# Optimization experiments

Measured on AMD Instinct MI355X. Metric: run time of the kernel, lower is better.

## Reference

```python
import jax, jax.numpy as jnp
import numpy as np

B, T, I, H, O = 128, 64, 512, 1024, 512
EPS = 0.01
N_MAX = 12  # static max ACT ponder steps per timestep (halts at ~2 steps at init)


def setup_inputs() -> dict:
    key = jax.random.key(0)
    ks = jax.random.split(key, 10)
    k = 1.0 / np.sqrt(H)
    u = lambda kk, shape: jax.random.uniform(kk, shape, jnp.float32, -k, k)
    return {
        "x": jax.random.normal(ks[0], (B, T, I), jnp.float32),
        "s0": jax.random.normal(ks[1], (1, B, H), jnp.float32) * 0.1,
        "w_ih": u(ks[2], (H, 1 + I)),
        "w_hh": u(ks[3], (H, H)),
        "b_ih": u(ks[4], (H,)),
        "b_hh": u(ks[5], (H,)),
        "w_halt": u(ks[6], (1, H)),
        "b_halt": u(ks[7], (1,)),
        "w_out": u(ks[8], (O, H)),
        "b_out": u(ks[9], (O,)),
    }


def _binarize_st(p):
    # Binarize autograd.Function: forward -> 1 where p > 0 (sigmoid outputs are
    # always positive, zeroed halted entries stay 0); backward -> identity (STE).
    return p + jax.lax.stop_gradient(jnp.where(p > 0, 1.0, 0.0) - p)


def reference(x, s0, w_ih, w_hh, b_ih, b_hh, w_halt, b_halt, w_out, b_out):
    def cell(inp, h):  # inp [B,1+I], h [B,H] -> tanh RNN cell
        return jnp.tanh(inp @ w_ih.T + b_ih + h @ w_hh.T + b_hh)

    def timestep(h_carry, x_t):  # h_carry [B,H], x_t [B,I]
        ones = jnp.ones((B, 1), x_t.dtype)
        x1 = jnp.concatenate([ones, x_t], axis=1)          # flag=1: first ponder step
        x0 = jnp.concatenate([ones * 0.0, x_t], axis=1)    # flag=0: continued pondering
        # ponder step 0 (always contributes for every sample)
        h = cell(x1, h_carry)
        out = h @ w_out.T + b_out                 # [B,O]
        p = jax.nn.sigmoid(h @ w_halt.T + b_halt) # [B,1]
        w = _binarize_st(p)
        out_acc = out * w
        h_acc = h * w
        cum = p[:, 0]
        # ponder value is only assigned when a sample halts at step 0 (original bug kept)
        pond = jnp.where(cum >= 1.0 - EPS, 2.0, 0.0)

        def ponder_step(carry, _):
            h_prev, cum, out_acc, h_acc = carry
            active = (cum < 1.0 - EPS).astype(h_prev.dtype)[:, None]  # [B,1]
            h = cell(x0, h_prev) * active
            out = (h @ w_out.T + b_out) * active
            p = jax.nn.sigmoid(h @ w_halt.T + b_halt) * active
            w = _binarize_st(p)
            return (h, cum + p[:, 0], out_acc + out * w, h_acc + h * w), None

        (h, cum, out_acc, h_acc), _ = jax.lax.scan(
            ponder_step, (h, cum, out_acc, h_acc), None, length=N_MAX - 1)
        # next-timestep hidden is the binarized-weight accumulation of states
        return h_acc, (out_acc, pond)

    h_last, (outputs, ponder) = jax.lax.scan(timestep, s0[0], jnp.swapaxes(x, 0, 1))
    return jnp.swapaxes(outputs, 0, 1), jnp.swapaxes(ponder, 0, 1)  # [B,T,O], [B,T]
```

## Files before the change

kernel.cpp:

```cpp
#include <hip/hip_runtime.h>
#include <hip/hip_cooperative_groups.h>
#include <math.h>

namespace cg = cooperative_groups;

#define NB 128
#define NT 64
#define NI 512
#define NH 1024
#define NO 512
#define PONDOFF (NB*NT*NO)

extern __shared__ float smem[];

__device__ __forceinline__ void group_barrier(unsigned* ctr, unsigned target, int tid)
{
    __syncthreads();
    if (tid == 0) {
        __hip_atomic_fetch_add(ctr, 1u, __ATOMIC_RELEASE, __HIP_MEMORY_SCOPE_AGENT);
        while (__hip_atomic_load(ctr, __ATOMIC_RELAXED, __HIP_MEMORY_SCOPE_AGENT) < target)
            __builtin_amdgcn_s_sleep(1);
    }
    if (tid < 64)
        __builtin_amdgcn_fence(__ATOMIC_ACQUIRE, "agent");
    __syncthreads();
}

__global__ void __launch_bounds__(1024, 1)
arnn_coop(const float* __restrict__ x, const float* __restrict__ s0,
          const float* __restrict__ w_ih, const float* __restrict__ w_hh,
          const float* __restrict__ b_ih, const float* __restrict__ b_hh,
          const float* __restrict__ w_halt, const float* __restrict__ b_halt,
          const float* __restrict__ w_out, const float* __restrict__ b_out,
          float* __restrict__ out, float* __restrict__ ws)
{
    cg::grid_group grid = cg::this_grid();
    const int tid = threadIdx.x;
    const int bid = blockIdx.x;
    const int gid = bid * 1024 + tid;

    float* wihT  = ws;
    float* hbuf  = wihT + NI*NH;
    float* habuf = hbuf + NB*2*NH;
    unsigned* ctrA = (unsigned*)(habuf + 2*NB*NH);

    const int gp = bid >> 5, lb = bid & 31;

    __shared__ float s_whalt[NH + (NH/16)*4];
    __shared__ int   s_t[16];
    __shared__ float s_cum[16];
    __shared__ int   s_n[16];
    __shared__ int   s_et[16], s_en[16];
    __shared__ unsigned char s_sl[16];
    __shared__ unsigned char s_run[16];
    __shared__ unsigned char s_mode[16];
    __shared__ unsigned char s_epi[16];

    for (int e = gid; e < NI*NH; e += 256*1024) {
        const int i = e >> 10, jj = e & 1023;
        wihT[e] = w_ih[jj*(NI+1) + 1 + i];
    }
    if (gid < 8*32)
        __hip_atomic_store(&ctrA[gid], 0u, __ATOMIC_RELAXED, __HIP_MEMORY_SCOPE_AGENT);
    for (int e = tid; e < 1024*32; e += 1024) {
        const int k = e & 1023, jj = e >> 10;
        const float v = w_hh[(lb*32 + jj)*NH + k];
        const int su = (jj >> 1) ^ ((k >> 6) & 15);
        smem[k*32 + su*2 + (jj & 1)] = v;
    }
    {
        const int j = tid;
        s_whalt[j + ((j >> 4) << 2)] = w_halt[j];
    }
    if (tid < 16) {
        s_t[tid] = 0; s_cum[tid] = 0.0f; s_n[tid] = 0;
        s_et[tid] = 0; s_en[tid] = 0;
        s_sl[tid] = 0; s_run[tid] = 1; s_mode[tid] = 0; s_epi[tid] = 0;
    }
    grid.sync();

    unsigned* ctr = ctrA + gp*32;

    const int w    = tid >> 6;
    const int lane = tid & 63;
    const int rq   = w >> 2;
    const int co   = w & 3;
    const int up   = lane & 3;
    const int ks   = lane >> 2;
    const int u    = co*4 + up;
    const int jg   = lb*32 + u*2;
    const int b0   = gp*16 + rq*4;
    const bool k0  = (ks == 0);
    const int ldsb = ks*2048 + ((u ^ ks) << 1);

    const float bh  = b_halt[0];
    const float bias0 = k0 ? (b_ih[jg]   + b_hh[jg])   : 0.0f;
    const float bias1 = k0 ? (b_ih[jg+1] + b_hh[jg+1]) : 0.0f;
    const float w0a   = k0 ? w_ih[jg*(NI+1)]     : 0.0f;
    const float w0b   = k0 ? w_ih[(jg+1)*(NI+1)] : 0.0f;

    const int   eo = lb*16 + (lane & 15);
    const int   eq = lane >> 4;
    const int   eb = gp*16 + w;
    const float bo = b_out[eo];

    auto decide_p = [&](int slot) -> float {
        const float* hr = hbuf + ((gp*16 + w)*2 + slot)*NH + lane*16;
        float d = 0.0f;
        #pragma unroll
        for (int q = 0; q < 16; q += 4) {
            const float4 hv = *(const float4*)(hr + q);
            const float4 wv = *(const float4*)(&s_whalt[lane*20 + q]);
            d += hv.x*wv.x + hv.y*wv.y + hv.z*wv.z + hv.w*wv.w;
        }
        d += __shfl_xor(d, 1);  d += __shfl_xor(d, 2);  d += __shfl_xor(d, 4);
        d += __shfl_xor(d, 8);  d += __shfl_xor(d, 16); d += __shfl_xor(d, 32);
        return 1.0f / (1.0f + expf(-(d + bh)));
    };

    float xw[4][2];
    float hacc[4][2];

    unsigned gen = 0;
    for (;;) {
        if (s_epi[w]) {
            const int et = s_et[w];
            const float* ha = habuf + (et&1)*(NB*NH) + eb*NH + eq*256;
            const float* wq = w_out + eo*NH + eq*256;
            float acc = 0.0f;
            #pragma unroll 4
            for (int jj2 = 0; jj2 < 256; jj2 += 4) {
                const float4 hv = *(const float4*)(ha + jj2);
                const float4 wv = *(const float4*)(wq + jj2);
                acc += hv.x*wv.x + hv.y*wv.y + hv.z*wv.z + hv.w*wv.w;
            }
            acc += __shfl_xor(acc, 16); acc += __shfl_xor(acc, 32);
            if (eq == 0) out[(eb*NT + et)*NO + eo] = acc + (float)s_en[w]*bo;
        }
        int ex[4], md[4], tt[4], sl[4];
        #pragma unroll
        for (int r = 0; r < 4; ++r) {
            const int rr = rq*4 + r;
            ex[r] = s_run[rr]; md[r] = s_mode[rr]; tt[r] = s_t[rr]; sl[r] = s_sl[rr];
        }
        if (ex[0] | ex[1] | ex[2] | ex[3]) {
            #pragma unroll
            for (int r = 0; r < 4; ++r) {
                if (ex[r] && md[r] == 0) {
                    float o0 = bias0, o1 = bias1;
                    const float* xr = x + ((b0+r)*NT + tt[r])*NI + ks*32;
                    const float* wp = wihT + (ks*32)*NH + jg;
                    #pragma unroll 4
                    for (int i = 0; i < 32; i += 4) {
                        const float4 xv = *(const float4*)(xr + i);
                        const float2 wa = *(const float2*)(wp + (i  )*NH);
                        const float2 wb = *(const float2*)(wp + (i+1)*NH);
                        const float2 wc = *(const float2*)(wp + (i+2)*NH);
                        const float2 wd = *(const float2*)(wp + (i+3)*NH);
                        o0 += xv.x*wa.x + xv.y*wb.x + xv.z*wc.x + xv.w*wd.x;
                        o1 += xv.x*wa.y + xv.y*wb.y + xv.z*wc.y + xv.w*wd.y;
                    }
                    xw[r][0] = o0; xw[r][1] = o1;
                }
            }
            float a[4][2];
            const float* hp[4];
            #pragma unroll
            for (int r = 0; r < 4; ++r) {
                const int b = b0 + r;
                a[r][0] = xw[r][0] + (md[r] == 0 ? w0a : 0.0f);
                a[r][1] = xw[r][1] + (md[r] == 0 ? w0b : 0.0f);
                if (!ex[r])           hp[r] = hbuf + (b*2)*NH + ks*64;
                else if (md[r] == 0)  hp[r] = (tt[r] == 0 ? s0 + b*NH
                                              : habuf + ((tt[r]-1)&1)*(NB*NH) + b*NH) + ks*64;
                else                  hp[r] = hbuf + (b*2 + sl[r])*NH + ks*64;
            }
            #pragma unroll 4
            for (int kc = 0; kc < 64; kc += 4) {
                const float4 h0 = *(const float4*)(hp[0] + kc);
                const float4 h1 = *(const float4*)(hp[1] + kc);
                const float4 h2 = *(const float4*)(hp[2] + kc);
                const float4 h3 = *(const float4*)(hp[3] + kc);
                const float2 wa = *(const float2*)(smem + ldsb + (kc  )*32);
                const float2 wb = *(const float2*)(smem + ldsb + (kc+1)*32);
                const float2 wc = *(const float2*)(smem + ldsb + (kc+2)*32);
                const float2 wd = *(const float2*)(smem + ldsb + (kc+3)*32);
                a[0][0] += h0.x*wa.x + h0.y*wb.x + h0.z*wc.x + h0.w*wd.x;
                a[0][1] += h0.x*wa.y + h0.y*wb.y + h0.z*wc.y + h0.w*wd.y;
                a[1][0] += h1.x*wa.x + h1.y*wb.x + h1.z*wc.x + h1.w*wd.x;
                a[1][1] += h1.x*wa.y + h1.y*wb.y + h1.z*wc.y + h1.w*wd.y;
                a[2][0] += h2.x*wa.x + h2.y*wb.x + h2.z*wc.x + h2.w*wd.x;
                a[2][1] += h2.x*wa.y + h2.y*wb.y + h2.z*wc.y + h2.w*wd.y;
                a[3][0] += h3.x*wa.x + h3.y*wb.x + h3.z*wc.x + h3.w*wd.x;
                a[3][1] += h3.x*wa.y + h3.y*wb.y + h3.z*wc.y + h3.w*wd.y;
            }
            #pragma unroll
            for (int r = 0; r < 4; ++r)
                #pragma unroll
                for (int c = 0; c < 2; ++c) {
                    float v = a[r][c];
                    v += __shfl_xor(v, 4);  v += __shfl_xor(v, 8);
                    v += __shfl_xor(v, 16); v += __shfl_xor(v, 32);
                    a[r][c] = v;
                }
            if (k0) {
                #pragma unroll
                for (int r = 0; r < 4; ++r) {
                    if (ex[r]) {
                        const float ha = tanhf(a[r][0]), hb = tanhf(a[r][1]);
                        const int b = b0 + r;
                        *(float2*)(hbuf + (b*2 + (sl[r]^1))*NH + jg) = make_float2(ha, hb);
                        if (md[r] == 0) { hacc[r][0] = ha;  hacc[r][1] = hb; }
                        else            { hacc[r][0] += ha; hacc[r][1] += hb; }
                        *(float2*)(habuf + (tt[r]&1)*(NB*NH) + b*NH + jg) =
                            make_float2(hacc[r][0], hacc[r][1]);
                    }
                }
            }
        }
        ++gen; group_barrier(ctr, 32*gen, tid);
        const int exw = s_run[w];
        float p = 0.0f;
        if (exw) p = decide_p(s_sl[w] ^ 1);
        if (lane == 0) {
            int newepi = 0;
            if (exw) {
                const int t = s_t[w];
                float cum; int n;
                if (s_mode[w] == 0) {
                    cum = p; n = 1;
                    if (lb == 0) out[PONDOFF + (gp*16 + w)*NT + t] = (p >= 0.99f) ? 2.0f : 0.0f;
                } else {
                    cum = s_cum[w] + p; n = s_n[w] + 1;
                }
                s_cum[w] = cum; s_n[w] = n;
                s_sl[w] ^= 1;
                if ((cum < 0.99f) && n < 12) {
                    s_mode[w] = 1;
                } else {
                    newepi = 1; s_et[w] = t; s_en[w] = n;
                    if (t == NT-1) s_run[w] = 0;
                    else { s_t[w] = t + 1; s_mode[w] = 0; }
                }
            }
            s_epi[w] = newepi;
        }
        __syncthreads();
        const int al = (lane < 16) ? (s_run[lane] | s_epi[lane]) : 0;
        if (__ballot(al) == 0ULL) break;
    }
}

extern "C" void kernel_launch(void* const* d_in, const int* in_sizes, int n_in,
                              void* d_out, int out_size, void* d_ws, size_t ws_size,
                              hipStream_t stream) {
    const float* x      = (const float*)d_in[0];
    const float* s0     = (const float*)d_in[1];
    const float* w_ih   = (const float*)d_in[2];
    const float* w_hh   = (const float*)d_in[3];
    const float* b_ih   = (const float*)d_in[4];
    const float* b_hh   = (const float*)d_in[5];
    const float* w_halt = (const float*)d_in[6];
    const float* b_halt = (const float*)d_in[7];
    const float* w_out  = (const float*)d_in[8];
    const float* b_out  = (const float*)d_in[9];
    float* out = (float*)d_out;
    float* ws  = (float*)d_ws;

    static const int kLds = 131072;
    hipFuncSetAttribute((const void*)arnn_coop,
                        hipFuncAttributeMaxDynamicSharedMemorySize, kLds);

    void* args[] = { (void*)&x, (void*)&s0, (void*)&w_ih, (void*)&w_hh,
                     (void*)&b_ih, (void*)&b_hh, (void*)&w_halt, (void*)&b_halt,
                     (void*)&w_out, (void*)&b_out, (void*)&out, (void*)&ws };
    hipLaunchCooperativeKernel((void*)arnn_coop, dim3(256), dim3(1024), args, kLds, stream);
}
```

Baseline: 9.415 ms.

## Replace grid-synchronized cooperative kernel with per-block batch-row independent kernel

```diff
diff --git a/kernel.cpp b/kernel.cpp
--- a/kernel.cpp
+++ b/kernel.cpp
@@ -1,8 +1,5 @@
 #include <hip/hip_runtime.h>
-#include <hip/hip_cooperative_groups.h>
 #include <math.h>
-
-namespace cg = cooperative_groups;
 
 #define NB 128
 #define NT 64
@@ -11,243 +8,230 @@
 #define NO 512
 #define PONDOFF (NB*NT*NO)
 
-extern __shared__ float smem[];
-
-__device__ __forceinline__ void group_barrier(unsigned* ctr, unsigned target, int tid)
+__device__ __forceinline__ int swz(int k) { return (k >> 7)*132 + (k & 127); }
+
+__global__ void prep_whhT(const float* __restrict__ w_hh, float* __restrict__ whhT)
 {
-    __syncthreads();
-    if (tid == 0) {
-        __hip_atomic_fetch_add(ctr, 1u, __ATOMIC_RELEASE, __HIP_MEMORY_SCOPE_AGENT);
-        while (__hip_atomic_load(ctr, __ATOMIC_RELAXED, __HIP_MEMORY_SCOPE_AGENT) < target)
-            __builtin_amdgcn_s_sleep(1);
+    int e = blockIdx.x*blockDim.x + threadIdx.x;
+    const int stride = gridDim.x*blockDim.x;
+    for (; e < NH*NH; e += stride) {
+        const int k = e >> 10, j = e & 1023;
+        whhT[e] = w_hh[j*NH + k];
     }
-    if (tid < 64)
-        __builtin_amdgcn_fence(__ATOMIC_ACQUIRE, "agent");
-    __syncthreads();
 }
 
-__global__ void __launch_bounds__(1024, 1)
-arnn_coop(const float* __restrict__ x, const float* __restrict__ s0,
-          const float* __restrict__ w_ih, const float* __restrict__ w_hh,
+__global__ void __launch_bounds__(1024)
+arnn_rows(const float* __restrict__ x, const float* __restrict__ s0,
+          const float* __restrict__ w_ih, const float* __restrict__ whhT,
           const float* __restrict__ b_ih, const float* __restrict__ b_hh,
           const float* __restrict__ w_halt, const float* __restrict__ b_halt,
           const float* __restrict__ w_out, const float* __restrict__ b_out,
-          float* __restrict__ out, float* __restrict__ ws)
+          float* __restrict__ out)
 {
-    cg::grid_group grid = cg::this_grid();
-    const int tid = threadIdx.x;
-    const int bid = blockIdx.x;
-    const int gid = bid * 1024 + tid;
-
-    float* wihT  = ws;
-    float* hbuf  = wihT + NI*NH;
-    float* habuf = hbuf + NB*2*NH;
-    unsigned* ctrA = (unsigned*)(habuf + 2*NB*NH);
-
-    const int gp = bid >> 5, lb = bid & 31;
-
-    __shared__ float s_whalt[NH + (NH/16)*4];
-    __shared__ int   s_t[16];
-    __shared__ float s_cum[16];
-    __shared__ int   s_n[16];
-    __shared__ int   s_et[16], s_en[16];
-    __shared__ unsigned char s_sl[16];
-    __shared__ unsigned char s_run[16];
-    __shared__ unsigned char s_mode[16];
-    __shared__ unsigned char s_epi[16];
-
-    for (int e = gid; e < NI*NH; e += 256*1024) {
-        const int i = e >> 10, jj = e & 1023;
-        wihT[e] = w_ih[jj*(NI+1) + 1 + i];
-    }
-    if (gid < 8*32)
-        __hip_atomic_store(&ctrA[gid], 0u, __ATOMIC_RELAXED, __HIP_MEMORY_SCOPE_AGENT);
-    for (int e = tid; e < 1024*32; e += 1024) {
-        const int k = e & 1023, jj = e >> 10;
-        const float v = w_hh[(lb*32 + jj)*NH + k];
-        const int su = (jj >> 1) ^ ((k >> 6) & 15);
-        smem[k*32 + su*2 + (jj & 1)] = v;
-    }
-    {
-        const int j = tid;
-        s_whalt[j + ((j >> 4) << 2)] = w_halt[j];
-    }
-    if (tid < 16) {
-        s_t[tid] = 0; s_cum[tid] = 0.0f; s_n[tid] = 0;
-        s_et[tid] = 0; s_en[tid] = 0;
-        s_sl[tid] = 0; s_run[tid] = 1; s_mode[tid] = 0; s_epi[tid] = 0;
-    }
-    grid.sync();
-
-    unsigned* ctr = ctrA + gp*32;
-
-    const int w    = tid >> 6;
+    const int tid  = threadIdx.x;
+    const int b0   = blockIdx.x * 2;
     const int lane = tid & 63;
-    const int rq   = w >> 2;
-    const int co   = w & 3;
-    const int up   = lane & 3;
-    const int ks   = lane >> 2;
-    const int u    = co*4 + up;
-    const int jg   = lb*32 + u*2;
-    const int b0   = gp*16 + rq*4;
-    const bool k0  = (ks == 0);
-    const int ldsb = ks*2048 + ((u ^ ks) << 1);
-
-    const float bh  = b_halt[0];
-    const float bias0 = k0 ? (b_ih[jg]   + b_hh[jg])   : 0.0f;
-    const float bias1 = k0 ? (b_ih[jg+1] + b_hh[jg+1]) : 0.0f;
-    const float w0a   = k0 ? w_ih[jg*(NI+1)]     : 0.0f;
-    const float w0b   = k0 ? w_ih[(jg+1)*(NI+1)] : 0.0f;
-
-    const int   eo = lb*16 + (lane & 15);
-    const int   eq = lane >> 4;
-    const int   eb = gp*16 + w;
-    const float bo = b_out[eo];
-
-    auto decide_p = [&](int slot) -> float {
-        const float* hr = hbuf + ((gp*16 + w)*2 + slot)*NH + lane*16;
-        float d = 0.0f;
-        #pragma unroll
-        for (int q = 0; q < 16; q += 4) {
-            const float4 hv = *(const float4*)(hr + q);
-            const float4 wv = *(const float4*)(&s_whalt[lane*20 + q]);
-            d += hv.x*wv.x + hv.y*wv.y + hv.z*wv.z + hv.w*wv.w;
-        }
-        d += __shfl_xor(d, 1);  d += __shfl_xor(d, 2);  d += __shfl_xor(d, 4);
-        d += __shfl_xor(d, 8);  d += __shfl_xor(d, 16); d += __shfl_xor(d, 32);
-        return 1.0f / (1.0f + expf(-(d + bh)));
-    };
-
-    float xw[4][2];
-    float hacc[4][2];
-
-    unsigned gen = 0;
-    for (;;) {
-        if (s_epi[w]) {
-            const int et = s_et[w];
-            const float* ha = habuf + (et&1)*(NB*NH) + eb*NH + eq*256;
-            const float* wq = w_out + eo*NH + eq*256;
-            float acc = 0.0f;
-            #pragma unroll 4
-            for (int jj2 = 0; jj2 < 256; jj2 += 4) {
-                const float4 hv = *(const float4*)(ha + jj2);
-                const float4 wv = *(const float4*)(wq + jj2);
-                acc += hv.x*wv.x + hv.y*wv.y + hv.z*wv.z + hv.w*wv.w;
-            }
-            acc += __shfl_xor(acc, 16); acc += __shfl_xor(acc, 32);
-            if (eq == 0) out[(eb*NT + et)*NO + eo] = acc + (float)s_en[w]*bo;
-        }
-        int ex[4], md[4], tt[4], sl[4];
-        #pragma unroll
-        for (int r = 0; r < 4; ++r) {
-            const int rr = rq*4 + r;
-            ex[r] = s_run[rr]; md[r] = s_mode[rr]; tt[r] = s_t[rr]; sl[r] = s_sl[rr];
-        }
-        if (ex[0] | ex[1] | ex[2] | ex[3]) {
-            #pragma unroll
-            for (int r = 0; r < 4; ++r) {
-                if (ex[r] && md[r] == 0) {
-                    float o0 = bias0, o1 = bias1;
-                    const float* xr = x + ((b0+r)*NT + tt[r])*NI + ks*32;
-                    const float* wp = wihT + (ks*32)*NH + jg;
-                    #pragma unroll 4
-                    for (int i = 0; i < 32; i += 4) {
-                        const float4 xv = *(const float4*)(xr + i);
-                        const float2 wa = *(const float2*)(wp + (i  )*NH);
-                        const float2 wb = *(const float2*)(wp + (i+1)*NH);
-                        const float2 wc = *(const float2*)(wp + (i+2)*NH);
-                        const float2 wd = *(const float2*)(wp + (i+3)*NH);
-                        o0 += xv.x*wa.x + xv.y*wb.x + xv.z*wc.x + xv.w*wd.x;
-                        o1 += xv.x*wa.y + xv.y*wb.y + xv.z*wc.y + xv.w*wd.y;
+    const int wv   = tid >> 6;
+    const int kq   = lane >> 3;
+    const int jp   = lane & 7;
+    const int j0   = wv*64 + jp*8;
+    const int g    = tid >> 4;
+    const int l16  = tid & 15;
+
+    __shared__ float s_h[2*2*1056];
+    __shared__ float s_xw[2*NH];
+    __shared__ float s_whalt[NH];
+    __shared__ float s_w0[NH];
+    __shared__ float s_bias[NH];
+    __shared__ float s_bout[NO];
+    __shared__ float s_pred[2][16][2];
+
+    s_whalt[tid] = w_halt[tid];
+    s_w0[tid]    = w_ih[tid*(NI+1)];
+    s_bias[tid]  = b_ih[tid] + b_hh[tid];
+    if (tid < NO) s_bout[tid] = b_out[tid];
+    s_h[swz(tid)]        = s0[(b0+0)*NH + tid];
+    s_h[1056 + swz(tid)] = s0[(b0+1)*NH + tid];
+    const float bh = b_halt[0];
+    __syncthreads();
+
+    int buf = 0;
+    float cum0 = 0.f, cum1 = 0.f;
+    int   en0 = 0, en1 = 0, act0 = 1, act1 = 1;
+
+    for (int t = 0; t < NT; ++t) {
+        {
+            float xa0[16], xa1[16];
+            #pragma unroll
+            for (int p = 0; p < 16; ++p) { xa0[p] = 0.f; xa1[p] = 0.f; }
+            const float* xr0 = x + ((b0+0)*NT + t)*NI + l16*32;
+            const float* xr1 = x + ((b0+1)*NT + t)*NI + l16*32;
+            for (int i2 = 0; i2 < 32; ++i2) {
+                const float xv0 = xr0[i2];
+                const float xv1 = xr1[i2];
+                const int   ib  = l16*32 + i2;
+                #pragma unroll
+                for (int p = 0; p < 16; ++p) {
+                    const float wvv = w_ih[(p*64 + g)*(NI+1) + 1 + ib];
+                    xa0[p] += wvv*xv0;
+                    xa1[p] += wvv*xv1;
+                }
+            }
+            #pragma unroll
+            for (int p = 0; p < 16; ++p) {
+                xa0[p] += __shfl_xor(xa0[p], 1); xa0[p] += __shfl_xor(xa0[p], 2);
+                xa0[p] += __shfl_xor(xa0[p], 4); xa0[p] += __shfl_xor(xa0[p], 8);
+                xa1[p] += __shfl_xor(xa1[p], 1); xa1[p] += __shfl_xor(xa1[p], 2);
+                xa1[p] += __shfl_xor(xa1[p], 4); xa1[p] += __shfl_xor(xa1[p], 8);
+            }
+            if (l16 == 0) {
+                #pragma unroll
+                for (int p = 0; p < 16; ++p) {
+                    const int j = p*64 + g;
+                    s_xw[j]      = xa0[p] + s_bias[j];
+                    s_xw[NH + j] = xa1[p] + s_bias[j];
+                }
+            }
+        }
+        __syncthreads();
+
+        float hacc0[8], hacc1[8];
+        act0 = 1; act1 = 1;
+        int n = 0;
+        for (;;) {
+            const int ismain = (n == 0);
+            float a0[8], a1[8];
+            #pragma unroll
+            for (int cc = 0; cc < 8; ++cc) { a0[cc] = 0.f; a1[cc] = 0.f; }
+            const float* hb0 = &s_h[(buf*2 + 0)*1056 + kq*132];
+            const float* hb1 = &s_h[(buf*2 + 1)*1056 + kq*132];
+            const float* wb  = whhT + (kq*128)*NH + j0;
+            #pragma unroll 2
+            for (int it4 = 0; it4 < 32; ++it4) {
+                const float4 hq0 = *(const float4*)(hb0 + it4*4);
+                const float4 hq1 = *(const float4*)(hb1 + it4*4);
+                const float h0c[4] = {hq0.x, hq0.y, hq0.z, hq0.w};
+                const float h1c[4] = {hq1.x, hq1.y, hq1.z, hq1.w};
+                #pragma unroll
+                for (int c = 0; c < 4; ++c) {
+                    const float4 wa  = *(const float4*)(wb + (it4*4 + c)*NH);
+                    const float4 wb4 = *(const float4*)(wb + (it4*4 + c)*NH + 4);
+                    const float wc8[8] = {wa.x, wa.y, wa.z, wa.w,
+                                          wb4.x, wb4.y, wb4.z, wb4.w};
+                    #pragma unroll
+                    for (int cc = 0; cc < 8; ++cc) {
+                        a0[cc] += wc8[cc]*h0c[c];
+                        a1[cc] += wc8[cc]*h1c[c];
                     }
-                    xw[r][0] = o0; xw[r][1] = o1;
-                }
-            }
-            float a[4][2];
-            const float* hp[4];
-            #pragma unroll
-            for (int r = 0; r < 4; ++r) {
-                const int b = b0 + r;
-                a[r][0] = xw[r][0] + (md[r] == 0 ? w0a : 0.0f);
-                a[r][1] = xw[r][1] + (md[r] == 0 ? w0b : 0.0f);
-                if (!ex[r])           hp[r] = hbuf + (b*2)*NH + ks*64;
-                else if (md[r] == 0)  hp[r] = (tt[r] == 0 ? s0 + b*NH
-                                              : habuf + ((tt[r]-1)&1)*(NB*NH) + b*NH) + ks*64;
-                else                  hp[r] = hbuf + (b*2 + sl[r])*NH + ks*64;
-            }
-            #pragma unroll 4
-            for (int kc = 0; kc < 64; kc += 4) {
-                const float4 h0 = *(const float4*)(hp[0] + kc);
-                const float4 h1 = *(const float4*)(hp[1] + kc);
-                const float4 h2 = *(const float4*)(hp[2] + kc);
-                const float4 h3 = *(const float4*)(hp[3] + kc);
-                const float2 wa = *(const float2*)(smem + ldsb + (kc  )*32);
-                const float2 wb = *(const float2*)(smem + ldsb + (kc+1)*32);
-                const float2 wc = *(const float2*)(smem + ldsb + (kc+2)*32);
-                const float2 wd = *(const float2*)(smem + ldsb + (kc+3)*32);
-                a[0][0] += h0.x*wa.x + h0.y*wb.x + h0.z*wc.x + h0.w*wd.x;
-                a[0][1] += h0.x*wa.y + h0.y*wb.y + h0.z*wc.y + h0.w*wd.y;
-                a[1][0] += h1.x*wa.x + h1.y*wb.x + h1.z*wc.x + h1.w*wd.x;
-                a[1][1] += h1.x*wa.y + h1.y*wb.y + h1.z*wc.y + h1.w*wd.y;
-                a[2][0] += h2.x*wa.x + h2.y*wb.x + h2.z*wc.x + h2.w*wd.x;
-                a[2][1] += h2.x*wa.y + h2.y*wb.y + h2.z*wc.y + h2.w*wd.y;
-                a[3][0] += h3.x*wa.x + h3.y*wb.x + h3.z*wc.x + h3.w*wd.x;
-                a[3][1] += h3.x*wa.y + h3.y*wb.y + h3.z*wc.y + h3.w*wd.y;
-            }
-            #pragma unroll
-            for (int r = 0; r < 4; ++r)
-                #pragma unroll
-                for (int c = 0; c < 2; ++c) {
-                    float v = a[r][c];
-                    v += __shfl_xor(v, 4);  v += __shfl_xor(v, 8);
-                    v += __shfl_xor(v, 16); v += __shfl_xor(v, 32);
-                    a[r][c] = v;
-                }
-            if (k0) {
-                #pragma unroll
-                for (int r = 0; r < 4; ++r) {
-                    if (ex[r]) {
-                        const float ha = tanhf(a[r][0]), hb = tanhf(a[r][1]);
-                        const int b = b0 + r;
-                        *(float2*)(hbuf + (b*2 + (sl[r]^1))*NH + jg) = make_float2(ha, hb);
-                        if (md[r] == 0) { hacc[r][0] = ha;  hacc[r][1] = hb; }
-                        else            { hacc[r][0] += ha; hacc[r][1] += hb; }
-                        *(float2*)(habuf + (tt[r]&1)*(NB*NH) + b*NH + jg) =
-                            make_float2(hacc[r][0], hacc[r][1]);
-                    }
-                }
-            }
-        }
-        ++gen; group_barrier(ctr, 32*gen, tid);
-        const int exw = s_run[w];
-        float p = 0.0f;
-        if (exw) p = decide_p(s_sl[w] ^ 1);
-        if (lane == 0) {
-            int newepi = 0;
-            if (exw) {
-                const int t = s_t[w];
-                float cum; int n;
-                if (s_mode[w] == 0) {
-                    cum = p; n = 1;
-                    if (lb == 0) out[PONDOFF + (gp*16 + w)*NT + t] = (p >= 0.99f) ? 2.0f : 0.0f;
-                } else {
-                    cum = s_cum[w] + p; n = s_n[w] + 1;
-                }
-                s_cum[w] = cum; s_n[w] = n;
-                s_sl[w] ^= 1;
-                if ((cum < 0.99f) && n < 12) {
-                    s_mode[w] = 1;
-                } else {
-                    newepi = 1; s_et[w] = t; s_en[w] = n;
-                    if (t == NT-1) s_run[w] = 0;
-                    else { s_t[w] = t + 1; s_mode[w] = 0; }
-                }
-            }
-            s_epi[w] = newepi;
+                }
+            }
+            #pragma unroll
+            for (int cc = 0; cc < 8; ++cc) {
+                a0[cc] += __shfl_xor(a0[cc], 8);
+                a0[cc] += __shfl_xor(a0[cc], 16);
+                a0[cc] += __shfl_xor(a0[cc], 32);
+                a1[cc] += __shfl_xor(a1[cc], 8);
+                a1[cc] += __shfl_xor(a1[cc], 16);
+                a1[cc] += __shfl_xor(a1[cc], 32);
+            }
+            float hn0[8], hn1[8];
+            float pp0 = 0.f, pp1 = 0.f;
+            #pragma unroll
+            for (int cc = 0; cc < 8; ++cc) {
+                const int j = j0 + cc;
+                float v0 = a0[cc] + s_xw[j];
+                float v1 = a1[cc] + s_xw[NH + j];
+                if (ismain) { v0 += s_w0[j]; v1 += s_w0[j]; }
+                hn0[cc] = act0 ? tanhf(v0) : 0.0f;
+                hn1[cc] = act1 ? tanhf(v1) : 0.0f;
+                pp0 += s_whalt[j]*hn0[cc];
+                pp1 += s_whalt[j]*hn1[cc];
+                if (ismain) { hacc0[cc] = hn0[cc];  hacc1[cc] = hn1[cc]; }
+                else        { hacc0[cc] += hn0[cc]; hacc1[cc] += hn1[cc]; }
+            }
+            pp0 += __shfl_xor(pp0, 1); pp0 += __shfl_xor(pp0, 2); pp0 += __shfl_xor(pp0, 4);
+            pp1 += __shfl_xor(pp1, 1); pp1 += __shfl_xor(pp1, 2); pp1 += __shfl_xor(pp1, 4);
+            if (lane == 0) { s_pred[n & 1][wv][0] = pp0; s_pred[n & 1][wv][1] = pp1; }
+            if (kq == 0) {
+                const int nb_ = buf ^ 1;
+                const int sa  = swz(j0);
+                float* d0 = &s_h[(nb_*2 + 0)*1056];
+                float* d1 = &s_h[(nb_*2 + 1)*1056];
+                *(float4*)(d0 + sa)     = make_float4(hn0[0], hn0[1], hn0[2], hn0[3]);
+                *(float4*)(d0 + sa + 4) = make_float4(hn0[4], hn0[5], hn0[6], hn0[7]);
+                *(float4*)(d1 + sa)     = make_float4(hn1[0], hn1[1], hn1[2], hn1[3]);
+                *(float4*)(d1 + sa + 4) = make_float4(hn1[4], hn1[5], hn1[6], hn1[7]);
+            }
+            __syncthreads();
+            float ps0 = 0.f, ps1 = 0.f;
+            #pragma unroll
+            for (int ww = 0; ww < 16; ++ww) {
+                ps0 += s_pred[n & 1][ww][0];
+                ps1 += s_pred[n & 1][ww][1];
+            }
+            const float p0 = act0 ? 1.0f/(1.0f + expf(-(ps0 + bh))) : 0.0f;
+            const float p1 = act1 ? 1.0f/(1.0f + expf(-(ps1 + bh))) : 0.0f;
+            if (ismain) {
+                cum0 = p0; cum1 = p1; en0 = 1; en1 = 1;
+                if (tid == 0) out[PONDOFF + (b0+0)*NT + t] = (p0 >= 0.99f) ? 2.0f : 0.0f;
+                if (tid == 1) out[PONDOFF + (b0+1)*NT + t] = (p1 >= 0.99f) ? 2.0f : 0.0f;
+            } else {
+                en0 += act0; en1 += act1;
+                cum0 += p0;  cum1 += p1;
+            }
+            act0 = (cum0 < 0.99f); act1 = (cum1 < 0.99f);
+            buf ^= 1;
+            ++n;
+            if (n == 12 || !(act0 | act1)) break;
+        }
+
+        const int hb2 = buf ^ 1;
+        if (kq == 0) {
+            const int sa = swz(j0);
+            float* d0 = &s_h[(hb2*2 + 0)*1056];
+            float* d1 = &s_h[(hb2*2 + 1)*1056];
+            *(float4*)(d0 + sa)     = make_float4(hacc0[0], hacc0[1], hacc0[2], hacc0[3]);
+            *(float4*)(d0 + sa + 4) = make_float4(hacc0[4], hacc0[5], hacc0[6], hacc0[7]);
+            *(float4*)(d1 + sa)     = make_float4(hacc1[0], hacc1[1], hacc1[2], hacc1[3]);
+            *(float4*)(d1 + sa + 4) = make_float4(hacc1[4], hacc1[5], hacc1[6], hacc1[7]);
         }
         __syncthreads();
-        const int al = (lane < 16) ? (s_run[lane] | s_epi[lane]) : 0;
-        if (__ballot(al) == 0ULL) break;
+        {
+            float e0[8], e1[8];
+            #pragma unroll
+            for (int p8 = 0; p8 < 8; ++p8) { e0[p8] = 0.f; e1[p8] = 0.f; }
+            const float* hs0 = &s_h[(hb2*2 + 0)*1056];
+            const float* hs1 = &s_h[(hb2*2 + 1)*1056];
+            #pragma unroll 2
+            for (int q = 0; q < 16; ++q) {
+                const int jj = l16*64 + q*4;
+                const int sa = swz(jj);
+                const float4 hv0 = *(const float4*)(hs0 + sa);
+                const float4 hv1 = *(const float4*)(hs1 + sa);
+                #pragma unroll
+                for (int p8 = 0; p8 < 8; ++p8) {
+                    const float4 wq = *(const float4*)(w_out + (p8*64 + g)*NH + jj);
+                    e0[p8] += wq.x*hv0.x + wq.y*hv0.y + wq.z*hv0.z + wq.w*hv0.w;
+                    e1[p8] += wq.x*hv1.x + wq.y*hv1.y + wq.z*hv1.z + wq.w*hv1.w;
+                }
+            }
+            #pragma unroll
+            for (int p8 = 0; p8 < 8; ++p8) {
+                e0[p8] += __shfl_xor(e0[p8], 1); e0[p8] += __shfl_xor(e0[p8], 2);
+                e0[p8] += __shfl_xor(e0[p8], 4); e0[p8] += __shfl_xor(e0[p8], 8);
+                e1[p8] += __shfl_xor(e1[p8], 1); e1[p8] += __shfl_xor(e1[p8], 2);
+                e1[p8] += __shfl_xor(e1[p8], 4); e1[p8] += __shfl_xor(e1[p8], 8);
+            }
+            if (l16 == 0) {
+                #pragma unroll
+                for (int p8 = 0; p8 < 8; ++p8) {
+                    const int o = p8*64 + g;
+                    out[((b0+0)*NT + t)*NO + o] = e0[p8] + (float)en0*s_bout[o];
+                    out[((b0+1)*NT + t)*NO + o] = e1[p8] + (float)en1*s_bout[o];
+                }
+            }
+        }
+        buf = hb2;
     }
 }
 
@@ -264,15 +248,11 @@
     const float* b_halt = (const float*)d_in[7];
     const float* w_out  = (const float*)d_in[8];
     const float* b_out  = (const float*)d_in[9];
-    float* out = (float*)d_out;
-    float* ws  = (float*)d_ws;
-
-    static const int kLds = 131072;
-    hipFuncSetAttribute((const void*)arnn_coop,
-                        hipFuncAttributeMaxDynamicSharedMemorySize, kLds);
-
-    void* args[] = { (void*)&x, (void*)&s0, (void*)&w_ih, (void*)&w_hh,
-                     (void*)&b_ih, (void*)&b_hh, (void*)&w_halt, (void*)&b_halt,
-                     (void*)&w_out, (void*)&b_out, (void*)&out, (void*)&ws };
-    hipLaunchCooperativeKernel((void*)arnn_coop, dim3(256), dim3(1024), args, kLds, stream);
+    float* out  = (float*)d_out;
+    float* whhT = (float*)d_ws;
+
+    hipLaunchKernelGGL(prep_whhT, dim3(256), dim3(1024), 0, stream, w_hh, whhT);
+    hipLaunchKernelGGL(arnn_rows, dim3(64), dim3(1024), 0, stream,
+                       x, s0, w_ih, whhT, b_ih, b_hh, w_halt, b_halt,
+                       w_out, b_out, out);
 }
```

After: 23.18 ms. +146.2%, slower.
